# Performance work log

Hardware: AMD Instinct MI355X
Metric: run time of the kernel (lower is better)

## Reference

```python
import jax, jax.numpy as jnp
import numpy as np

NUM_NODES = 200000
NUM_EDGES = 1250000
DIM = 64
K_LAYERS = 3
BATCH = 4096
CAND = 101  # 1 positive + 100 negatives


def setup_inputs() -> dict:
    key = jax.random.key(0)
    k1, k2, k3 = jax.random.split(key, 3)
    emb = jax.random.normal(k1, (NUM_NODES, DIM), dtype=jnp.float32)
    edge_index = jax.random.randint(k2, (2, NUM_EDGES), 0, NUM_NODES)
    batch = jax.random.randint(k3, (BATCH, CAND, 3), 0, NUM_NODES)
    return {"emb": emb, "edge_index": edge_index, "batch": batch,
            "num_nodes": NUM_NODES}


def reference(emb, edge_index, batch, num_nodes):
    # --- LightGCN.get_embedding: K rounds of symmetric-normalized SpMM ---
    row, col = edge_index[0], edge_index[1]  # source -> target
    ones = jnp.ones(row.shape[0], dtype=emb.dtype)
    deg = jax.ops.segment_sum(ones, col, num_segments=num_nodes)  # in-degree
    deg_safe = jnp.where(deg > 0, deg, 1.0)
    dis = jnp.where(deg > 0, jax.lax.rsqrt(deg_safe), 0.0)  # deg^{-1/2}, inf->0
    norm = dis[row] * dis[col]  # [E]

    alpha = 1.0 / (K_LAYERS + 1)  # uniform layer combination
    x = emb
    out = x * alpha
    for _ in range(K_LAYERS):
        # propagate: out[i] = sum_{(j->i)} norm_e * x[j]
        x = jax.ops.segment_sum(x[row] * norm[:, None], col,
                                num_segments=num_nodes)
        out = out + x * alpha

    # --- scoring: gather user/item embeddings, elementwise dot ---
    user_idx = batch[:, :, 0].reshape(-1)
    item_idx = batch[:, :, 1].reshape(-1)
    logits = jnp.sum(out[user_idx] * out[item_idx], axis=-1)  # [B*CAND]
    return logits.reshape(batch.shape[0], -1)
```

## Files before the change

### kernel.cpp

```cpp
#include <hip/hip_runtime.h>

#define DIM 64
#define BSHIFT 8
#define MAXNB 1024
#define CHUNK 4096
#define EPT (CHUNK / 256)

__device__ inline unsigned packbf(float a, float b) {
    unsigned ua = __float_as_uint(a), ub = __float_as_uint(b);
    unsigned ra = (ua + 0x7FFFu + ((ua >> 16) & 1u)) >> 16;
    unsigned rb = (ub + 0x7FFFu + ((ub >> 16) & 1u)) >> 16;
    return ra | (rb << 16);
}
__device__ inline void unpackbf(unsigned u, float& lo, float& hi) {
    lo = __uint_as_float(u << 16);
    hi = __uint_as_float(u & 0xFFFF0000u);
}
__device__ inline void acc_row(const uint4 v, float* s) {
    float lo, hi;
    unpackbf(v.x, lo, hi); s[0] += lo; s[1] += hi;
    unpackbf(v.y, lo, hi); s[2] += lo; s[3] += hi;
    unpackbf(v.z, lo, hi); s[4] += lo; s[5] += hi;
    unpackbf(v.w, lo, hi); s[6] += lo; s[7] += hi;
}
__device__ inline void acc_row_m(const uint4 v, float m, float* s) {
    float lo, hi;
    unpackbf(v.x, lo, hi); s[0] = fmaf(m, lo, s[0]); s[1] = fmaf(m, hi, s[1]);
    unpackbf(v.y, lo, hi); s[2] = fmaf(m, lo, s[2]); s[3] = fmaf(m, hi, s[3]);
    unpackbf(v.z, lo, hi); s[4] = fmaf(m, lo, s[4]); s[5] = fmaf(m, hi, s[5]);
    unpackbf(v.w, lo, hi); s[6] = fmaf(m, lo, s[6]); s[7] = fmaf(m, hi, s[7]);
}

__global__ __launch_bounds__(256) void block_hist_kernel(
        const int* __restrict__ col, int* __restrict__ H, int E, int NB,
        int nblocks) {
    __shared__ int h[MAXNB];
    int tid = threadIdx.x;
    for (int k = tid; k < NB; k += 256) h[k] = 0;
    __syncthreads();
    int base = blockIdx.x * CHUNK;
    #pragma unroll
    for (int k = 0; k < EPT; k++) {
        int e = base + tid + k * 256;
        if (e < E) atomicAdd(&h[col[e] >> BSHIFT], 1);
    }
    __syncthreads();
    for (int k = tid; k < NB; k += 256) H[(size_t)k * nblocks + blockIdx.x] = h[k];
}

__global__ void scan_tile_sum_kernel(const int* __restrict__ H,
                                     int* __restrict__ T, int M) {
    int tid = threadIdx.x;
    int base = blockIdx.x * 1024 + tid * 4;
    int s = 0;
    #pragma unroll
    for (int k = 0; k < 4; k++)
        if (base + k < M) s += H[base + k];
    __shared__ int lds[256];
    lds[tid] = s;
    __syncthreads();
    for (int off = 128; off > 0; off >>= 1) {
        if (tid < off) lds[tid] += lds[tid + off];
        __syncthreads();
    }
    if (tid == 0) T[blockIdx.x] = lds[0];
}

__global__ void scan_tile_offsets_kernel(int* __restrict__ T, int nt) {
    __shared__ int lds[256];
    int tid = threadIdx.x;
    int v = (tid < nt) ? T[tid] : 0;
    lds[tid] = v;
    __syncthreads();
    for (int off = 1; off < 256; off <<= 1) {
        int t = (tid >= off) ? lds[tid - off] : 0;
        __syncthreads();
        lds[tid] += t;
        __syncthreads();
    }
    if (tid < nt) T[tid] = lds[tid] - v;
}

__global__ void scan_final_kernel(const int* __restrict__ H,
                                  const int* __restrict__ T,
                                  int* __restrict__ S,
                                  int* __restrict__ bbase, int M, int nblocks,
                                  int NB, int E) {
    int tid = threadIdx.x;
    int base = blockIdx.x * 1024 + tid * 4;
    int c[4];
    int local = 0;
    #pragma unroll
    for (int k = 0; k < 4; k++) {
        c[k] = (base + k < M) ? H[base + k] : 0;
        local += c[k];
    }
    __shared__ int lds[256];
    lds[tid] = local;
    __syncthreads();
    for (int off = 1; off < 256; off <<= 1) {
        int t = (tid >= off) ? lds[tid - off] : 0;
        __syncthreads();
        lds[tid] += t;
        __syncthreads();
    }
    int excl = lds[tid] - local + T[blockIdx.x];
    #pragma unroll
    for (int k = 0; k < 4; k++) {
        int idx = base + k;
        if (idx < M) {
            S[idx] = excl;
            if (idx % nblocks == 0) bbase[idx / nblocks] = excl;
        }
        excl += c[k];
    }
    if (blockIdx.x == 0 && tid == 0) bbase[NB] = E;
}

__global__ __launch_bounds__(256) void scatter_binned_kernel(
        const int* __restrict__ row, const int* __restrict__ col,
        const int* __restrict__ S, unsigned* __restrict__ pairs, int E,
        int NB, int nblocks) {
    __shared__ unsigned stage[CHUNK];
    __shared__ int gdst[CHUNK];
    __shared__ int hist[MAXNB];
    __shared__ int pfx[MAXNB];
    __shared__ int gbase[MAXNB];
    int tid = threadIdx.x;
    int bid = blockIdx.x;
    int base = bid * CHUNK;
    int nloc = min(CHUNK, E - base);

    for (int b = tid; b < NB; b += 256) hist[b] = 0;
    __syncthreads();

    unsigned vals[EPT];
    int keys[EPT];
    #pragma unroll
    for (int k = 0; k < EPT; k++) {
        int e = base + tid + k * 256;
        if (e < E) {
            int d = col[e];
            int s = row[e];
            keys[k] = d >> BSHIFT;
            vals[k] = (unsigned)s | ((unsigned)(d & 255) << 24);
            atomicAdd(&hist[keys[k]], 1);
        } else {
            keys[k] = -1;
        }
    }
    __syncthreads();

    int b0 = tid * 4;
    int c4[4];
    int loc = 0;
    #pragma unroll
    for (int k = 0; k < 4; k++) {
        c4[k] = (b0 + k < NB) ? hist[b0 + k] : 0;
        loc += c4[k];
    }
    gbase[tid] = loc;
    __syncthreads();
    for (int off = 1; off < 256; off <<= 1) {
        int t = (tid >= off) ? gbase[tid - off] : 0;
        __syncthreads();
        gbase[tid] += t;
        __syncthreads();
    }
    int excl = gbase[tid] - loc;
    #pragma unroll
    for (int k = 0; k < 4; k++) {
        if (b0 + k < NB) pfx[b0 + k] = excl;
        excl += c4[k];
    }
    __syncthreads();

    for (int b = tid; b < NB; b += 256) {
        gbase[b] = S[(size_t)b * nblocks + bid];
        hist[b] = pfx[b];
    }
    __syncthreads();

    #pragma unroll
    for (int k = 0; k < EPT; k++) {
        if (keys[k] >= 0) {
            int slot = atomicAdd(&hist[keys[k]], 1);
            stage[slot] = vals[k];
            gdst[slot] = gbase[keys[k]] + (slot - pfx[keys[k]]);
        }
    }
    __syncthreads();

    for (int s = tid; s < nloc; s += 256) pairs[gdst[s]] = stage[s];
}

__global__ __launch_bounds__(256) void fine_fill_kernel(
        const unsigned* __restrict__ pairs, const int* __restrict__ bbase,
        int* __restrict__ row_ptr, int* __restrict__ csr_src,
        const float4* __restrict__ emb4, uint4* __restrict__ z4, int N,
        int E) {
    __shared__ int cnt[256];
    __shared__ int cur[256];
    __shared__ float wds[256];
    int b = blockIdx.x;
    int tid = threadIdx.x;
    int beg = bbase[b], end = bbase[b + 1];
    cnt[tid] = 0;
    __syncthreads();
    for (int j = beg + tid; j < end; j += 256)
        atomicAdd(&cnt[pairs[j] >> 24], 1);
    __syncthreads();
    int v = cnt[tid];
    wds[tid] = (v > 0) ? rsqrtf((float)v) : 0.0f;
    for (int off = 1; off < 256; off <<= 1) {
        int t = (tid >= off) ? cnt[tid - off] : 0;
        __syncthreads();
        cnt[tid] += t;
        __syncthreads();
    }
    int excl = cnt[tid] - v;
    int node0 = (b << BSHIFT) + tid;
    if (node0 < N) row_ptr[node0] = beg + excl;
    cur[tid] = beg + excl;
    __syncthreads();
    for (int j = beg + tid; j < end; j += 256) {
        unsigned p = pairs[j];
        int pos = atomicAdd(&cur[p >> 24], 1);
        csr_src[pos] = (int)(p & 0xFFFFFFu);
    }
    if (b == 0 && tid == 0) row_ptr[N] = E;

    int gl = tid & 7;
    #pragma unroll
    for (int g = 0; g < 8; g++) {
        int il = g * 32 + (tid >> 3);
        int node = (b << BSHIFT) + il;
        if (node < N) {
            float wd = wds[il];
            size_t eo = (size_t)node * 16 + gl * 2;
            float4 a = emb4[eo], c = emb4[eo + 1];
            uint4 z;
            z.x = packbf(a.x * wd, a.y * wd);
            z.y = packbf(a.z * wd, a.w * wd);
            z.z = packbf(c.x * wd, c.y * wd);
            z.w = packbf(c.z * wd, c.w * wd);
            z4[(size_t)node * 8 + gl] = z;
        }
    }
}

__device__ inline void row_gather_sum(const int* __restrict__ csr_src,
                                      const uint4* __restrict__ z4, int b,
                                      int e, int gl, float* s) {
    if (b >= e) return;
    int e1 = e - 1;
    int j = b;
    int i0 = csr_src[j];
    int i1 = csr_src[min(j + 1, e1)];
    int i2 = csr_src[min(j + 2, e1)];
    int i3 = csr_src[min(j + 3, e1)];
    while (j < e) {
        uint4 v0 = z4[(size_t)i0 * 8 + gl];
        uint4 v1 = z4[(size_t)i1 * 8 + gl];
        uint4 v2 = z4[(size_t)i2 * 8 + gl];
        uint4 v3 = z4[(size_t)i3 * 8 + gl];
        int jn = j + 4;
        if (jn < e) {
            i0 = csr_src[jn];
            i1 = csr_src[min(jn + 1, e1)];
            i2 = csr_src[min(jn + 2, e1)];
            i3 = csr_src[min(jn + 3, e1)];
        }
        float m1 = (j + 1 < e) ? 1.0f : 0.0f;
        float m2 = (j + 2 < e) ? 1.0f : 0.0f;
        float m3 = (j + 3 < e) ? 1.0f : 0.0f;
        acc_row(v0, s);
        acc_row_m(v1, m1, s);
        acc_row_m(v2, m2, s);
        acc_row_m(v3, m3, s);
        j = jn;
    }
}

__global__ __launch_bounds__(256) void spmm_pull_kernel(
        const int* __restrict__ row_ptr, const int* __restrict__ csr_src,
        const uint4* __restrict__ z4, uint4* __restrict__ znext4, int N) {
    int t = blockIdx.x * blockDim.x + threadIdx.x;
    int i = t >> 3;
    int gl = t & 7;
    if (i >= N) return;
    int b = row_ptr[i], e = row_ptr[i + 1];
    float s[8] = {0, 0, 0, 0, 0, 0, 0, 0};
    row_gather_sum(csr_src, z4, b, e, gl, s);
    int deg = e - b;
    float wd = (deg > 0) ? rsqrtf((float)deg) : 0.0f;
    float w2 = wd * wd;
    uint4 z;
    z.x = packbf(s[0] * w2, s[1] * w2);
    z.y = packbf(s[2] * w2, s[3] * w2);
    z.z = packbf(s[4] * w2, s[5] * w2);
    z.w = packbf(s[6] * w2, s[7] * w2);
    znext4[(size_t)i * 8 + gl] = z;
}

__global__ __launch_bounds__(256) void spmm_combine_kernel(
        const int* __restrict__ row_ptr, const int* __restrict__ csr_src,
        const uint4* __restrict__ z2, const uint4* __restrict__ z1,
        const float4* __restrict__ emb4, uint4* __restrict__ accb, int N) {
    int t = blockIdx.x * blockDim.x + threadIdx.x;
    int i = t >> 3;
    int gl = t & 7;
    if (i >= N) return;
    int b = row_ptr[i], e = row_ptr[i + 1];
    float s[8] = {0, 0, 0, 0, 0, 0, 0, 0};
    row_gather_sum(csr_src, z2, b, e, gl, s);
    int deg = e - b;
    float wd = (deg > 0) ? rsqrtf((float)deg) : 0.0f;
    float sq = (deg > 0) ? sqrtf((float)deg) : 0.0f;
    size_t zo = (size_t)i * 8 + gl;
    uint4 a1 = z1[zo], a2 = z2[zo];
    float w[8] = {0, 0, 0, 0, 0, 0, 0, 0};
    acc_row(a1, w); acc_row(a2, w);
    size_t eo = (size_t)i * 16 + gl * 2;
    float4 e0 = emb4[eo], e1 = emb4[eo + 1];
    float r0 = e0.x + sq * w[0] + wd * s[0];
    float r1 = e0.y + sq * w[1] + wd * s[1];
    float r2 = e0.z + sq * w[2] + wd * s[2];
    float r3 = e0.w + sq * w[3] + wd * s[3];
    float r4 = e1.x + sq * w[4] + wd * s[4];
    float r5 = e1.y + sq * w[5] + wd * s[5];
    float r6 = e1.z + sq * w[6] + wd * s[6];
    float r7 = e1.w + sq * w[7] + wd * s[7];
    uint4 z;
    z.x = packbf(r0, r1);
    z.y = packbf(r2, r3);
    z.z = packbf(r4, r5);
    z.w = packbf(r6, r7);
    accb[zo] = z;
}

__global__ __launch_bounds__(256) void score_kernel(
        const int* __restrict__ batch, const uint4* __restrict__ accb,
        float* __restrict__ out, int P) {
    int t = blockIdx.x * blockDim.x + threadIdx.x;
    int p = t >> 3;
    int gl = t & 7;
    if (p >= P) return;
    int u = batch[(size_t)p * 3 + 0];
    int it = batch[(size_t)p * 3 + 1];
    uint4 a = accb[(size_t)u * 8 + gl];
    uint4 b = accb[(size_t)it * 8 + gl];
    float sa[8] = {0, 0, 0, 0, 0, 0, 0, 0};
    float sb[8] = {0, 0, 0, 0, 0, 0, 0, 0};
    acc_row(a, sa);
    acc_row(b, sb);
    float s = sa[0] * sb[0] + sa[1] * sb[1] + sa[2] * sb[2] + sa[3] * sb[3] +
              sa[4] * sb[4] + sa[5] * sb[5] + sa[6] * sb[6] + sa[7] * sb[7];
    s += __shfl_xor(s, 4, 64);
    s += __shfl_xor(s, 2, 64);
    s += __shfl_xor(s, 1, 64);
    if (gl == 0) out[p] = s * 0.0625f;
}

extern "C" void kernel_launch(void* const* d_in, const int* in_sizes, int n_in,
                              void* d_out, int out_size, void* d_ws,
                              size_t ws_size, hipStream_t stream) {
    const float* emb = (const float*)d_in[0];
    const int* edge_index = (const int*)d_in[1];
    const int* batch = (const int*)d_in[2];
    float* out = (float*)d_out;

    const int N = in_sizes[0] / DIM;
    const int E = in_sizes[1] / 2;
    const int P = out_size;
    const int NB = (N + 255) >> BSHIFT;
    const int nblocks = (E + CHUNK - 1) / CHUNK;
    const int M = NB * nblocks;
    const int nt = (M + 1023) / 1024;

    const int* row = edge_index;
    const int* col = edge_index + E;

    const size_t zbytes = (size_t)N * DIM * 2;

    auto align256 = [](size_t x) { return (x + 255) & ~(size_t)255; };
    char* ws = (char*)d_ws;
    uint4* z0   = (uint4*)ws; ws += align256(zbytes);
    uint4* z1   = (uint4*)ws; ws += align256(zbytes);
    uint4* z2   = (uint4*)ws; ws += align256(zbytes);
    uint4* accb = (uint4*)ws; ws += align256(zbytes);
    unsigned* pairs = (unsigned*)ws; ws += align256((size_t)E * 4);
    int* csr_src    = (int*)ws;      ws += align256((size_t)E * 4);
    int* row_ptr    = (int*)ws;      ws += align256((size_t)(N + 1) * 4);
    int* H          = (int*)ws;      ws += align256((size_t)M * 4);
    int* S          = (int*)ws;      ws += align256((size_t)M * 4);
    int* T          = (int*)ws;      ws += align256(256 * 4);
    int* bbase      = (int*)ws;

    block_hist_kernel<<<nblocks, 256, 0, stream>>>(col, H, E, NB, nblocks);
    scan_tile_sum_kernel<<<nt, 256, 0, stream>>>(H, T, M);
    scan_tile_offsets_kernel<<<1, 256, 0, stream>>>(T, nt);
    scan_final_kernel<<<nt, 256, 0, stream>>>(H, T, S, bbase, M, nblocks, NB, E);
    scatter_binned_kernel<<<nblocks, 256, 0, stream>>>(row, col, S, pairs, E,
                                                       NB, nblocks);
    fine_fill_kernel<<<NB, 256, 0, stream>>>(pairs, bbase, row_ptr, csr_src,
                                             (const float4*)emb, z0, N, E);

    const int nodeBlocks = (N * 8 + 255) / 256;

    spmm_pull_kernel<<<nodeBlocks, 256, 0, stream>>>(row_ptr, csr_src, z0, z1, N);
    spmm_pull_kernel<<<nodeBlocks, 256, 0, stream>>>(row_ptr, csr_src, z1, z2, N);
    spmm_combine_kernel<<<nodeBlocks, 256, 0, stream>>>(row_ptr, csr_src, z2,
                                                        z1, (const float4*)emb,
                                                        accb, N);

    score_kernel<<<(P * 8 + 255) / 256, 256, 0, stream>>>(batch, accb, out, P);
}
```

Measured before the change: 249.9 us.

## Process SpMM rows in degree-sorted order to reduce wavefront divergence

Builds a degree histogram during CSR construction, scans it, and produces a permutation of nodes grouped by in-degree. The SpMM pull and combine kernels then take their rows from that permutation, so the 8 rows in a wavefront have similar gather loop lengths and divergence is reduced. This costs two extra small kernels and an extra indirection, and it scatters output writes and row_ptr reads, which loses the coalescing and locality the natural node order had.

After: 283.5 us. 1.13x slower.

```diff
diff --git a/kernel.cpp b/kernel.cpp
--- a/kernel.cpp
+++ b/kernel.cpp
@@ -5,6 +5,7 @@
 #define MAXNB 1024
 #define CHUNK 4096
 #define EPT (CHUNK / 256)
+#define DBINS 64
 
 __device__ inline unsigned packbf(float a, float b) {
     unsigned ua = __float_as_uint(a), ub = __float_as_uint(b);
@@ -66,9 +67,11 @@
     if (tid == 0) T[blockIdx.x] = lds[0];
 }
 
-__global__ void scan_tile_offsets_kernel(int* __restrict__ T, int nt) {
+__global__ void scan_tile_offsets_kernel(int* __restrict__ T, int nt,
+                                         int* __restrict__ dhist) {
     __shared__ int lds[256];
     int tid = threadIdx.x;
+    if (tid < DBINS) dhist[tid] = 0;
     int v = (tid < nt) ? T[tid] : 0;
     lds[tid] = v;
     __syncthreads();
@@ -197,21 +200,25 @@
 __global__ __launch_bounds__(256) void fine_fill_kernel(
         const unsigned* __restrict__ pairs, const int* __restrict__ bbase,
         int* __restrict__ row_ptr, int* __restrict__ csr_src,
-        const float4* __restrict__ emb4, uint4* __restrict__ z4, int N,
-        int E) {
+        const float4* __restrict__ emb4, uint4* __restrict__ z4,
+        int* __restrict__ dhist, int N, int E) {
     __shared__ int cnt[256];
     __shared__ int cur[256];
     __shared__ float wds[256];
+    __shared__ int dh[DBINS];
     int b = blockIdx.x;
     int tid = threadIdx.x;
     int beg = bbase[b], end = bbase[b + 1];
     cnt[tid] = 0;
+    if (tid < DBINS) dh[tid] = 0;
     __syncthreads();
     for (int j = beg + tid; j < end; j += 256)
         atomicAdd(&cnt[pairs[j] >> 24], 1);
     __syncthreads();
     int v = cnt[tid];
     wds[tid] = (v > 0) ? rsqrtf((float)v) : 0.0f;
+    int node0 = (b << BSHIFT) + tid;
+    if (node0 < N) atomicAdd(&dh[min(v, DBINS - 1)], 1);
     for (int off = 1; off < 256; off <<= 1) {
         int t = (tid >= off) ? cnt[tid - off] : 0;
         __syncthreads();
@@ -219,10 +226,10 @@
         __syncthreads();
     }
     int excl = cnt[tid] - v;
-    int node0 = (b << BSHIFT) + tid;
     if (node0 < N) row_ptr[node0] = beg + excl;
     cur[tid] = beg + excl;
     __syncthreads();
+    if (tid < DBINS && dh[tid] > 0) atomicAdd(&dhist[tid], dh[tid]);
     for (int j = beg + tid; j < end; j += 256) {
         unsigned p = pairs[j];
         int pos = atomicAdd(&cur[p >> 24], 1);
@@ -246,6 +253,42 @@
             z.w = packbf(c.z * wd, c.w * wd);
             z4[(size_t)node * 8 + gl] = z;
         }
+    }
+}
+
+__global__ void dscan_kernel(const int* __restrict__ dhist,
+                             int* __restrict__ dcursor) {
+    if (threadIdx.x == 0) {
+        int acc = 0;
+        for (int k = 0; k < DBINS; k++) {
+            dcursor[k] = acc;
+            acc += dhist[k];
+        }
+    }
+}
+
+__global__ __launch_bounds__(256) void perm_kernel(
+        const int* __restrict__ row_ptr, int* __restrict__ dcursor,
+        int* __restrict__ perm, int N) {
+    __shared__ int lh[DBINS];
+    __shared__ int lbase[DBINS];
+    __shared__ int lcur[DBINS];
+    int tid = threadIdx.x;
+    int node = blockIdx.x * 256 + tid;
+    int bin = -1;
+    if (node < N) {
+        int deg = row_ptr[node + 1] - row_ptr[node];
+        bin = min(deg, DBINS - 1);
+    }
+    if (tid < DBINS) { lh[tid] = 0; lcur[tid] = 0; }
+    __syncthreads();
+    if (bin >= 0) atomicAdd(&lh[bin], 1);
+    __syncthreads();
+    if (tid < DBINS && lh[tid] > 0) lbase[tid] = atomicAdd(&dcursor[tid], lh[tid]);
+    __syncthreads();
+    if (bin >= 0) {
+        int r = atomicAdd(&lcur[bin], 1);
+        perm[lbase[bin] + r] = node;
     }
 }
 
@@ -283,12 +326,14 @@
 }
 
 __global__ __launch_bounds__(256) void spmm_pull_kernel(
-        const int* __restrict__ row_ptr, const int* __restrict__ csr_src,
-        const uint4* __restrict__ z4, uint4* __restrict__ znext4, int N) {
+        const int* __restrict__ perm, const int* __restrict__ row_ptr,
+        const int* __restrict__ csr_src, const uint4* __restrict__ z4,
+        uint4* __restrict__ znext4, int N) {
     int t = blockIdx.x * blockDim.x + threadIdx.x;
-    int i = t >> 3;
+    int g = t >> 3;
     int gl = t & 7;
-    if (i >= N) return;
+    if (g >= N) return;
+    int i = perm[g];
     int b = row_ptr[i], e = row_ptr[i + 1];
     float s[8] = {0, 0, 0, 0, 0, 0, 0, 0};
     row_gather_sum(csr_src, z4, b, e, gl, s);
@@ -304,13 +349,15 @@
 }
 
 __global__ __launch_bounds__(256) void spmm_combine_kernel(
-        const int* __restrict__ row_ptr, const int* __restrict__ csr_src,
-        const uint4* __restrict__ z2, const uint4* __restrict__ z1,
-        const float4* __restrict__ emb4, uint4* __restrict__ accb, int N) {
+        const int* __restrict__ perm, const int* __restrict__ row_ptr,
+        const int* __restrict__ csr_src, const uint4* __restrict__ z2,
+        const uint4* __restrict__ z1, const float4* __restrict__ emb4,
+        uint4* __restrict__ accb, int N) {
     int t = blockIdx.x * blockDim.x + threadIdx.x;
-    int i = t >> 3;
+    int g = t >> 3;
     int gl = t & 7;
-    if (i >= N) return;
+    if (g >= N) return;
+    int i = perm[g];
     int b = row_ptr[i], e = row_ptr[i + 1];
     float s[8] = {0, 0, 0, 0, 0, 0, 0, 0};
     row_gather_sum(csr_src, z2, b, e, gl, s);
@@ -392,26 +439,36 @@
     unsigned* pairs = (unsigned*)ws; ws += align256((size_t)E * 4);
     int* csr_src    = (int*)ws;      ws += align256((size_t)E * 4);
     int* row_ptr    = (int*)ws;      ws += align256((size_t)(N + 1) * 4);
+    int* perm       = (int*)ws;      ws += align256((size_t)N * 4);
     int* H          = (int*)ws;      ws += align256((size_t)M * 4);
     int* S          = (int*)ws;      ws += align256((size_t)M * 4);
     int* T          = (int*)ws;      ws += align256(256 * 4);
-    int* bbase      = (int*)ws;
+    int* bbase      = (int*)ws;      ws += align256((size_t)(NB + 1) * 4);
+    int* dhist      = (int*)ws;      ws += align256(DBINS * 4);
+    int* dcursor    = (int*)ws;
 
     block_hist_kernel<<<nblocks, 256, 0, stream>>>(col, H, E, NB, nblocks);
     scan_tile_sum_kernel<<<nt, 256, 0, stream>>>(H, T, M);
-    scan_tile_offsets_kernel<<<1, 256, 0, stream>>>(T, nt);
+    scan_tile_offsets_kernel<<<1, 256, 0, stream>>>(T, nt, dhist);
     scan_final_kernel<<<nt, 256, 0, stream>>>(H, T, S, bbase, M, nblocks, NB, E);
     scatter_binned_kernel<<<nblocks, 256, 0, stream>>>(row, col, S, pairs, E,
                                                        NB, nblocks);
     fine_fill_kernel<<<NB, 256, 0, stream>>>(pairs, bbase, row_ptr, csr_src,
-                                             (const float4*)emb, z0, N, E);
+                                             (const float4*)emb, z0, dhist,
+                                             N, E);
+
+    dscan_kernel<<<1, 64, 0, stream>>>(dhist, dcursor);
+    perm_kernel<<<(N + 255) / 256, 256, 0, stream>>>(row_ptr, dcursor, perm, N);
 
     const int nodeBlocks = (N * 8 + 255) / 256;
 
-    spmm_pull_kernel<<<nodeBlocks, 256, 0, stream>>>(row_ptr, csr_src, z0, z1, N);
-    spmm_pull_kernel<<<nodeBlocks, 256, 0, stream>>>(row_ptr, csr_src, z1, z2, N);
-    spmm_combine_kernel<<<nodeBlocks, 256, 0, stream>>>(row_ptr, csr_src, z2,
-                                                        z1, (const float4*)emb,
+    spmm_pull_kernel<<<nodeBlocks, 256, 0, stream>>>(perm, row_ptr, csr_src,
+                                                     z0, z1, N);
+    spmm_pull_kernel<<<nodeBlocks, 256, 0, stream>>>(perm, row_ptr, csr_src,
+                                                     z1, z2, N);
+    spmm_combine_kernel<<<nodeBlocks, 256, 0, stream>>>(perm, row_ptr, csr_src,
+                                                        z2, z1,
+                                                        (const float4*)emb,
                                                         accb, N);
 
     score_kernel<<<(P * 8 + 255) / 256, 256, 0, stream>>>(batch, accb, out, P);
```
